# Optimization experiments

Hardware: AMD Instinct MI355X
Metric: run time of the kernel (lower is better)

Reference implementation:

```python
import jax, jax.numpy as jnp
import numpy as np

B, N, C, K = 1024, 100, 256, 3  # batch, num_proposals, hidden_dim, conv kernel size
LN_EPS = 1e-5


def setup_inputs() -> dict:
    key = jax.random.key(0)
    k1, k2, k3 = jax.random.split(key, 3)
    query = jax.random.normal(k1, (B, N, C), dtype=jnp.float32)
    value = jax.random.normal(k2, (B, N, C), dtype=jnp.float32)
    # weight_linear: Linear(hidden_dim -> kernel_size)
    W_w = jax.random.normal(k3, (K, C), dtype=jnp.float32) * (1.0 / np.sqrt(C))
    b_w = jnp.zeros((K,), dtype=jnp.float32)
    # LayerNorm(hidden_dim)
    gamma = jnp.ones((C,), dtype=jnp.float32)
    beta = jnp.zeros((C,), dtype=jnp.float32)
    return {"query": query, "value": value, "W_w": W_w, "b_w": b_w,
            "gamma": gamma, "beta": beta}


def reference(query, value, W_w, b_w, gamma, beta):
    Bq, Nq, Cq = query.shape
    Kk = W_w.shape[0]
    # dynamic depthwise kernels: [B, N, K]
    w = jnp.einsum('bnc,kc->bnk', query, W_w) + b_w
    # torch conv1d with padding='same' (cross-correlation along C, groups=N)
    pad_l = (Kk - 1) // 2
    pad_r = Kk // 2
    vpad = jnp.pad(value, ((0, 0), (0, 0), (pad_l, pad_r)))
    # sliding windows along channel axis: [B, N, C, K]
    win = jnp.stack([vpad[:, :, k:k + Cq] for k in range(Kk)], axis=-1)
    out = jnp.einsum('bnck,bnk->bnc', win, w)
    # LayerNorm over last dim
    mu = jnp.mean(out, axis=-1, keepdims=True)
    var = jnp.mean(jnp.square(out - mu), axis=-1, keepdims=True)
    out = (out - mu) * jax.lax.rsqrt(var + LN_EPS) * gamma + beta
    return out
```

## Files before the change

### kernel.cpp

```cpp
#include <hip/hip_runtime.h>

constexpr int B = 1024, N = 100, C = 256, K = 3;
constexpr int ROWS = B * N;
constexpr int WAVES_PER_BLOCK = 4;
constexpr int BLOCKS = ROWS / WAVES_PER_BLOCK;
constexpr float LN_EPS = 1e-5f;

__global__ __launch_bounds__(256) void dydwconv_ln_kernel(
    const float* __restrict__ query,
    const float* __restrict__ value,
    const float* __restrict__ Ww,
    const float* __restrict__ bw,
    const float* __restrict__ gamma,
    const float* __restrict__ beta,
    float* __restrict__ out)
{
    __shared__ float sW[K * C];
    __shared__ float sGamma[C];
    __shared__ float sBeta[C];
    __shared__ float sBw[K];

    const int t = threadIdx.x;
    sW[t]         = Ww[t];
    sW[t + C]     = Ww[t + C];
    sW[t + 2 * C] = Ww[t + 2 * C];
    sGamma[t] = gamma[t];
    sBeta[t]  = beta[t];
    if (t < K) sBw[t] = bw[t];
    __syncthreads();

    const int wave = t >> 6;
    const int lane = t & 63;
    const int row  = blockIdx.x * WAVES_PER_BLOCK + wave;

    const size_t base = (size_t)row * C + lane * 4;
    const float4 q4 = *(const float4*)(query + base);
    const float4 v4 = *(const float4*)(value + base);

    const int c0 = lane * 4;
    float p0 = q4.x * sW[c0]         + q4.y * sW[c0 + 1]         + q4.z * sW[c0 + 2]         + q4.w * sW[c0 + 3];
    float p1 = q4.x * sW[C + c0]     + q4.y * sW[C + c0 + 1]     + q4.z * sW[C + c0 + 2]     + q4.w * sW[C + c0 + 3];
    float p2 = q4.x * sW[2*C + c0]   + q4.y * sW[2*C + c0 + 1]   + q4.z * sW[2*C + c0 + 2]   + q4.w * sW[2*C + c0 + 3];

    #pragma unroll
    for (int off = 32; off > 0; off >>= 1) {
        p0 += __shfl_xor(p0, off);
        p1 += __shfl_xor(p1, off);
        p2 += __shfl_xor(p2, off);
    }
    const float w0 = p0 + sBw[0];
    const float w1 = p1 + sBw[1];
    const float w2 = p2 + sBw[2];

    float vleft  = __shfl_up(v4.w, 1);
    float vright = __shfl_down(v4.x, 1);
    if (lane == 0)  vleft  = 0.0f;
    if (lane == 63) vright = 0.0f;

    const float o0 = vleft * w0 + v4.x * w1 + v4.y * w2;
    const float o1 = v4.x  * w0 + v4.y * w1 + v4.z * w2;
    const float o2 = v4.y  * w0 + v4.z * w1 + v4.w * w2;
    const float o3 = v4.z  * w0 + v4.w * w1 + vright * w2;

    float s  = o0 + o1 + o2 + o3;
    float ss = o0 * o0 + o1 * o1 + o2 * o2 + o3 * o3;
    #pragma unroll
    for (int off = 32; off > 0; off >>= 1) {
        s  += __shfl_xor(s, off);
        ss += __shfl_xor(ss, off);
    }
    const float mu  = s * (1.0f / C);
    const float var = ss * (1.0f / C) - mu * mu;
    const float inv = rsqrtf(var + LN_EPS);

    float4 r;
    r.x = (o0 - mu) * inv * sGamma[c0]     + sBeta[c0];
    r.y = (o1 - mu) * inv * sGamma[c0 + 1] + sBeta[c0 + 1];
    r.z = (o2 - mu) * inv * sGamma[c0 + 2] + sBeta[c0 + 2];
    r.w = (o3 - mu) * inv * sGamma[c0 + 3] + sBeta[c0 + 3];
    *(float4*)(out + base) = r;
}

extern "C" void kernel_launch(void* const* d_in, const int* in_sizes, int n_in,
                              void* d_out, int out_size, void* d_ws, size_t ws_size,
                              hipStream_t stream) {
    const float* query = (const float*)d_in[0];
    const float* value = (const float*)d_in[1];
    const float* Ww    = (const float*)d_in[2];
    const float* bw    = (const float*)d_in[3];
    const float* gamma = (const float*)d_in[4];
    const float* beta  = (const float*)d_in[5];
    float* out = (float*)d_out;

    dydwconv_ln_kernel<<<BLOCKS, 256, 0, stream>>>(query, value, Ww, bw, gamma, beta, out);
}
```

Before: 255.7 us.

## Process four rows per wave, reuse weights in registers, use nontemporal stores

Each wave now handles four rows instead of one. The per-block shared-memory setup (weights, gamma, beta) is amortized over 16 rows, the weight and gamma/beta values are hoisted into registers, and the shuffle reductions are interleaved across rows for more ILP. Output is written with nontemporal stores to avoid polluting cache. This costs more registers per thread and launches fewer blocks.

Result: no change. 260.7 us (+1.9%).

```diff
diff --git a/kernel.cpp b/kernel.cpp
--- a/kernel.cpp
+++ b/kernel.cpp
@@ -2,9 +2,13 @@
 
 constexpr int B = 1024, N = 100, C = 256, K = 3;
 constexpr int ROWS = B * N;
+constexpr int ROWS_PER_WAVE = 4;
 constexpr int WAVES_PER_BLOCK = 4;
-constexpr int BLOCKS = ROWS / WAVES_PER_BLOCK;
+constexpr int ROWS_PER_BLOCK = ROWS_PER_WAVE * WAVES_PER_BLOCK;
+constexpr int BLOCKS = ROWS / ROWS_PER_BLOCK;
 constexpr float LN_EPS = 1e-5f;
+
+typedef float nfloat4 __attribute__((ext_vector_type(4)));
 
 __global__ __launch_bounds__(256) void dydwconv_ln_kernel(
     const float* __restrict__ query,
@@ -18,7 +22,6 @@
     __shared__ float sW[K * C];
     __shared__ float sGamma[C];
     __shared__ float sBeta[C];
-    __shared__ float sBw[K];
 
     const int t = threadIdx.x;
     sW[t]         = Ww[t];
@@ -26,59 +29,86 @@
     sW[t + 2 * C] = Ww[t + 2 * C];
     sGamma[t] = gamma[t];
     sBeta[t]  = beta[t];
-    if (t < K) sBw[t] = bw[t];
     __syncthreads();
 
     const int wave = t >> 6;
     const int lane = t & 63;
-    const int row  = blockIdx.x * WAVES_PER_BLOCK + wave;
+    const int c0   = lane * 4;
+    const int row0 = (blockIdx.x * WAVES_PER_BLOCK + wave) * ROWS_PER_WAVE;
 
-    const size_t base = (size_t)row * C + lane * 4;
-    const float4 q4 = *(const float4*)(query + base);
-    const float4 v4 = *(const float4*)(value + base);
+    float4 q[ROWS_PER_WAVE], v[ROWS_PER_WAVE];
+    #pragma unroll
+    for (int r = 0; r < ROWS_PER_WAVE; ++r) {
+        const size_t base = (size_t)(row0 + r) * C + c0;
+        q[r] = *(const float4*)(query + base);
+        v[r] = *(const float4*)(value + base);
+    }
 
-    const int c0 = lane * 4;
-    float p0 = q4.x * sW[c0]         + q4.y * sW[c0 + 1]         + q4.z * sW[c0 + 2]         + q4.w * sW[c0 + 3];
-    float p1 = q4.x * sW[C + c0]     + q4.y * sW[C + c0 + 1]     + q4.z * sW[C + c0 + 2]     + q4.w * sW[C + c0 + 3];
-    float p2 = q4.x * sW[2*C + c0]   + q4.y * sW[2*C + c0 + 1]   + q4.z * sW[2*C + c0 + 2]   + q4.w * sW[2*C + c0 + 3];
+    const float W0a = sW[c0],       W0b = sW[c0+1],       W0c = sW[c0+2],       W0d = sW[c0+3];
+    const float W1a = sW[C+c0],     W1b = sW[C+c0+1],     W1c = sW[C+c0+2],     W1d = sW[C+c0+3];
+    const float W2a = sW[2*C+c0],   W2b = sW[2*C+c0+1],   W2c = sW[2*C+c0+2],   W2d = sW[2*C+c0+3];
+
+    float p[ROWS_PER_WAVE][K];
+    #pragma unroll
+    for (int r = 0; r < ROWS_PER_WAVE; ++r) {
+        p[r][0] = q[r].x * W0a + q[r].y * W0b + q[r].z * W0c + q[r].w * W0d;
+        p[r][1] = q[r].x * W1a + q[r].y * W1b + q[r].z * W1c + q[r].w * W1d;
+        p[r][2] = q[r].x * W2a + q[r].y * W2b + q[r].z * W2c + q[r].w * W2d;
+    }
+    #pragma unroll
+    for (int off = 32; off > 0; off >>= 1) {
+        #pragma unroll
+        for (int r = 0; r < ROWS_PER_WAVE; ++r) {
+            p[r][0] += __shfl_xor(p[r][0], off);
+            p[r][1] += __shfl_xor(p[r][1], off);
+            p[r][2] += __shfl_xor(p[r][2], off);
+        }
+    }
+    const float bw0 = bw[0], bw1 = bw[1], bw2 = bw[2];
+
+    float o[ROWS_PER_WAVE][4];
+    float s[ROWS_PER_WAVE], ss[ROWS_PER_WAVE];
+    #pragma unroll
+    for (int r = 0; r < ROWS_PER_WAVE; ++r) {
+        const float w0 = p[r][0] + bw0;
+        const float w1 = p[r][1] + bw1;
+        const float w2 = p[r][2] + bw2;
+        float vl = __shfl_up(v[r].w, 1);
+        float vr = __shfl_down(v[r].x, 1);
+        if (lane == 0)  vl = 0.0f;
+        if (lane == 63) vr = 0.0f;
+        o[r][0] = vl     * w0 + v[r].x * w1 + v[r].y * w2;
+        o[r][1] = v[r].x * w0 + v[r].y * w1 + v[r].z * w2;
+        o[r][2] = v[r].y * w0 + v[r].z * w1 + v[r].w * w2;
+        o[r][3] = v[r].z * w0 + v[r].w * w1 + vr     * w2;
+        s[r]  = o[r][0] + o[r][1] + o[r][2] + o[r][3];
+        ss[r] = o[r][0]*o[r][0] + o[r][1]*o[r][1] + o[r][2]*o[r][2] + o[r][3]*o[r][3];
+    }
+    #pragma unroll
+    for (int off = 32; off > 0; off >>= 1) {
+        #pragma unroll
+        for (int r = 0; r < ROWS_PER_WAVE; ++r) {
+            s[r]  += __shfl_xor(s[r],  off);
+            ss[r] += __shfl_xor(ss[r], off);
+        }
+    }
+
+    const float g0 = sGamma[c0], g1 = sGamma[c0+1], g2 = sGamma[c0+2], g3 = sGamma[c0+3];
+    const float be0 = sBeta[c0], be1 = sBeta[c0+1], be2 = sBeta[c0+2], be3 = sBeta[c0+3];
 
     #pragma unroll
-    for (int off = 32; off > 0; off >>= 1) {
-        p0 += __shfl_xor(p0, off);
-        p1 += __shfl_xor(p1, off);
-        p2 += __shfl_xor(p2, off);
+    for (int r = 0; r < ROWS_PER_WAVE; ++r) {
+        const float mu  = s[r] * (1.0f / C);
+        const float var = ss[r] * (1.0f / C) - mu * mu;
+        const float inv = rsqrtf(var + LN_EPS);
+        nfloat4 res;
+        res.x = (o[r][0] - mu) * inv * g0 + be0;
+        res.y = (o[r][1] - mu) * inv * g1 + be1;
+        res.z = (o[r][2] - mu) * inv * g2 + be2;
+        res.w = (o[r][3] - mu) * inv * g3 + be3;
+        const size_t base = (size_t)(row0 + r) * C + c0;
+        __builtin_nontemporal_store(res, (nfloat4*)(out + base));
     }
-    const float w0 = p0 + sBw[0];
-    const float w1 = p1 + sBw[1];
-    const float w2 = p2 + sBw[2];
-
-    float vleft  = __shfl_up(v4.w, 1);
-    float vright = __shfl_down(v4.x, 1);
-    if (lane == 0)  vleft  = 0.0f;
-    if (lane == 63) vright = 0.0f;
-
-    const float o0 = vleft * w0 + v4.x * w1 + v4.y * w2;
-    const float o1 = v4.x  * w0 + v4.y * w1 + v4.z * w2;
-    const float o2 = v4.y  * w0 + v4.z * w1 + v4.w * w2;
-    const float o3 = v4.z  * w0 + v4.w * w1 + vright * w2;
-
-    float s  = o0 + o1 + o2 + o3;
-    float ss = o0 * o0 + o1 * o1 + o2 * o2 + o3 * o3;
-    #pragma unroll
-    for (int off = 32; off > 0; off >>= 1) {
-        s  += __shfl_xor(s, off);
-        ss += __shfl_xor(ss, off);
-    }
-    const float mu  = s * (1.0f / C);
-    const float var = ss * (1.0f / C) - mu * mu;
-    const float inv = rsqrtf(var + LN_EPS);
-
-    float4 r;
-    r.x = (o0 - mu) * inv * sGamma[c0]     + sBeta[c0];
-    r.y = (o1 - mu) * inv * sGamma[c0 + 1] + sBeta[c0 + 1];
-    r.z = (o2 - mu) * inv * sGamma[c0 + 2] + sBeta[c0 + 2];
-    r.w = (o3 - mu) * inv * sGamma[c0 + 3] + sBeta[c0 + 3];
-    *(float4*)(out + base) = r;
 }
 
 extern "C" void kernel_launch(void* const* d_in, const int* in_sizes, int n_in,
```

## Process four rows per wave with sixteen channels per lane and nontemporal stores

Applied to the files above, without the earlier changes.

Each wave now handles four rows, with 16 lanes per row and 16 contiguous channels per lane, instead of one row per wave with 4 channels per lane. This cuts the shuffle-reduction depth from six steps to four, reads the weight, gamma and beta values from shared memory as vectors, and spreads the per-block setup cost (loading the weights, barrier) over four times as many rows. Output writes use nontemporal stores to avoid polluting cache. The trade-offs are higher register pressure, a quarter as many blocks, and lane loads with a 64-byte stride that may coalesce less cleanly.

After: 353.6 us. 38.3% more time.

```diff
diff --git a/kernel.cpp b/kernel.cpp
--- a/kernel.cpp
+++ b/kernel.cpp
@@ -2,9 +2,15 @@
 
 constexpr int B = 1024, N = 100, C = 256, K = 3;
 constexpr int ROWS = B * N;
+constexpr int LANES_PER_ROW = 16;
+constexpr int CH_PER_LANE = 16;
+constexpr int ROWS_PER_WAVE = 4;
 constexpr int WAVES_PER_BLOCK = 4;
-constexpr int BLOCKS = ROWS / WAVES_PER_BLOCK;
+constexpr int ROWS_PER_BLOCK = ROWS_PER_WAVE * WAVES_PER_BLOCK;
+constexpr int BLOCKS = ROWS / ROWS_PER_BLOCK;
 constexpr float LN_EPS = 1e-5f;
+
+typedef float nfloat4 __attribute__((ext_vector_type(4)));
 
 __global__ __launch_bounds__(256) void dydwconv_ln_kernel(
     const float* __restrict__ query,
@@ -18,7 +24,6 @@
     __shared__ float sW[K * C];
     __shared__ float sGamma[C];
     __shared__ float sBeta[C];
-    __shared__ float sBw[K];
 
     const int t = threadIdx.x;
     sW[t]         = Ww[t];
@@ -26,59 +31,81 @@
     sW[t + 2 * C] = Ww[t + 2 * C];
     sGamma[t] = gamma[t];
     sBeta[t]  = beta[t];
-    if (t < K) sBw[t] = bw[t];
     __syncthreads();
 
     const int wave = t >> 6;
     const int lane = t & 63;
-    const int row  = blockIdx.x * WAVES_PER_BLOCK + wave;
+    const int l    = lane & (LANES_PER_ROW - 1);
+    const int sub  = lane >> 4;
+    const int row  = (blockIdx.x * WAVES_PER_BLOCK + wave) * ROWS_PER_WAVE + sub;
+    const int c0   = l * CH_PER_LANE;
 
-    const size_t base = (size_t)row * C + lane * 4;
-    const float4 q4 = *(const float4*)(query + base);
-    const float4 v4 = *(const float4*)(value + base);
+    const size_t base = (size_t)row * C + c0;
 
-    const int c0 = lane * 4;
-    float p0 = q4.x * sW[c0]         + q4.y * sW[c0 + 1]         + q4.z * sW[c0 + 2]         + q4.w * sW[c0 + 3];
-    float p1 = q4.x * sW[C + c0]     + q4.y * sW[C + c0 + 1]     + q4.z * sW[C + c0 + 2]     + q4.w * sW[C + c0 + 3];
-    float p2 = q4.x * sW[2*C + c0]   + q4.y * sW[2*C + c0 + 1]   + q4.z * sW[2*C + c0 + 2]   + q4.w * sW[2*C + c0 + 3];
+    nfloat4 q4[4], v4[4];
+    #pragma unroll
+    for (int j = 0; j < 4; ++j) {
+        q4[j] = *(const nfloat4*)(query + base + 4 * j);
+        v4[j] = *(const nfloat4*)(value + base + 4 * j);
+    }
 
+    float p0 = 0.f, p1 = 0.f, p2 = 0.f;
     #pragma unroll
-    for (int off = 32; off > 0; off >>= 1) {
+    for (int j = 0; j < 4; ++j) {
+        const nfloat4 qq = q4[j];
+        const nfloat4 a = *(const nfloat4*)(sW + c0 + 4 * j);
+        const nfloat4 b = *(const nfloat4*)(sW + C + c0 + 4 * j);
+        const nfloat4 c = *(const nfloat4*)(sW + 2 * C + c0 + 4 * j);
+        p0 += qq.x * a.x + qq.y * a.y + qq.z * a.z + qq.w * a.w;
+        p1 += qq.x * b.x + qq.y * b.y + qq.z * b.z + qq.w * b.w;
+        p2 += qq.x * c.x + qq.y * c.y + qq.z * c.z + qq.w * c.w;
+    }
+    #pragma unroll
+    for (int off = 8; off > 0; off >>= 1) {
         p0 += __shfl_xor(p0, off);
         p1 += __shfl_xor(p1, off);
         p2 += __shfl_xor(p2, off);
     }
-    const float w0 = p0 + sBw[0];
-    const float w1 = p1 + sBw[1];
-    const float w2 = p2 + sBw[2];
+    const float w0 = p0 + bw[0];
+    const float w1 = p1 + bw[1];
+    const float w2 = p2 + bw[2];
 
-    float vleft  = __shfl_up(v4.w, 1);
-    float vright = __shfl_down(v4.x, 1);
-    if (lane == 0)  vleft  = 0.0f;
-    if (lane == 63) vright = 0.0f;
+    float vl = __shfl_up(v4[3].w, 1);
+    float vr = __shfl_down(v4[0].x, 1);
+    if (l == 0)                  vl = 0.0f;
+    if (l == LANES_PER_ROW - 1)  vr = 0.0f;
 
-    const float o0 = vleft * w0 + v4.x * w1 + v4.y * w2;
-    const float o1 = v4.x  * w0 + v4.y * w1 + v4.z * w2;
-    const float o2 = v4.y  * w0 + v4.z * w1 + v4.w * w2;
-    const float o3 = v4.z  * w0 + v4.w * w1 + vright * w2;
-
-    float s  = o0 + o1 + o2 + o3;
-    float ss = o0 * o0 + o1 * o1 + o2 * o2 + o3 * o3;
+    float o[CH_PER_LANE];
+    float s = 0.f, ss = 0.f;
     #pragma unroll
-    for (int off = 32; off > 0; off >>= 1) {
-        s  += __shfl_xor(s, off);
+    for (int j = 0; j < CH_PER_LANE; ++j) {
+        const float left  = (j == 0)  ? vl : v4[(j - 1) >> 2][(j - 1) & 3];
+        const float mid   = v4[j >> 2][j & 3];
+        const float right = (j == 15) ? vr : v4[(j + 1) >> 2][(j + 1) & 3];
+        o[j] = left * w0 + mid * w1 + right * w2;
+        s  += o[j];
+        ss += o[j] * o[j];
+    }
+    #pragma unroll
+    for (int off = 8; off > 0; off >>= 1) {
+        s  += __shfl_xor(s,  off);
         ss += __shfl_xor(ss, off);
     }
     const float mu  = s * (1.0f / C);
     const float var = ss * (1.0f / C) - mu * mu;
     const float inv = rsqrtf(var + LN_EPS);
 
-    float4 r;
-    r.x = (o0 - mu) * inv * sGamma[c0]     + sBeta[c0];
-    r.y = (o1 - mu) * inv * sGamma[c0 + 1] + sBeta[c0 + 1];
-    r.z = (o2 - mu) * inv * sGamma[c0 + 2] + sBeta[c0 + 2];
-    r.w = (o3 - mu) * inv * sGamma[c0 + 3] + sBeta[c0 + 3];
-    *(float4*)(out + base) = r;
+    #pragma unroll
+    for (int j = 0; j < 4; ++j) {
+        const nfloat4 g  = *(const nfloat4*)(sGamma + c0 + 4 * j);
+        const nfloat4 be = *(const nfloat4*)(sBeta  + c0 + 4 * j);
+        nfloat4 res;
+        res.x = (o[4 * j + 0] - mu) * inv * g.x + be.x;
+        res.y = (o[4 * j + 1] - mu) * inv * g.y + be.y;
+        res.z = (o[4 * j + 2] - mu) * inv * g.z + be.z;
+        res.w = (o[4 * j + 3] - mu) * inv * g.w + be.w;
+        __builtin_nontemporal_store(res, (nfloat4*)(out + base + 4 * j));
+    }
 }
 
 extern "C" void kernel_launch(void* const* d_in, const int* in_sizes, int n_in,
```
